# Optimization experiments

Hardware: AMD Instinct MI355X
Metric: run time of the kernel (lower is better)

Reference implementation:

```python
import jax, jax.numpy as jnp
import numpy as np

NUM_SINK = 8   # cfg.SINKHORN_ITERS
MASS = 0.9     # marginal value used for a and b


def _graph_conv(x, W_enc, b_enc, W1, b1, W2, b2, k):
    # Node encoder
    h = jax.nn.relu(x @ W_enc + b_enc)                       # [G,M,D]
    # kNN in embedding space (per graph)
    sq = jnp.sum(h * h, axis=-1)                             # [G,M]
    d2 = sq[:, :, None] + sq[:, None, :] - 2.0 * jnp.einsum('gmd,gnd->gmn', h, h)
    d2 = d2 + jnp.eye(h.shape[1], dtype=h.dtype) * 1e9       # exclude self-loop
    _, idx = jax.lax.top_k(-d2, k)                           # [G,M,k]
    neigh = jax.vmap(lambda hg, ig: hg[ig])(h, idx)          # [G,M,k,D]
    hc = jnp.broadcast_to(h[:, :, None, :], neigh.shape)
    e = jnp.concatenate([hc, neigh - hc], axis=-1)           # [G,M,k,2D]
    e = jax.nn.relu(e @ W1 + b1)                             # edge embed
    e = e @ W2 + b2                                          # back to D
    return jnp.max(e, axis=2)                                # max-aggregate over neighbors


def _sinkhorn(cost, lam):
    # log-domain unrolled Sinkhorn, batched over graphs; a=b=0.9 marginals
    log_p = -cost / lam                                      # [G,M,N]
    log_m = jnp.log(jnp.asarray(MASS, cost.dtype))
    for _ in range(NUM_SINK - 1):
        log_p = log_p - (jax.nn.logsumexp(log_p, axis=2, keepdims=True) - log_m)
        log_p = log_p - (jax.nn.logsumexp(log_p, axis=1, keepdims=True) - log_m)
    log_p = log_p - (jax.nn.logsumexp(log_p, axis=2, keepdims=True) - log_m)
    return jnp.exp(log_p)


def setup_inputs() -> dict:
    key = jax.random.key(0)
    ks = jax.random.split(key, 6)
    G, M, D = 64, 256, 256
    E = 256  # edge embed size
    inp = {
        'tra_x': jax.random.normal(ks[0], (G, M, D), jnp.float32),
        'det_x': jax.random.normal(ks[1], (G, M, D), jnp.float32),
        'W_enc': jax.random.normal(ks[2], (D, D), jnp.float32) / np.sqrt(D),
        'b_enc': jnp.zeros((D,), jnp.float32),
        'W1': jax.random.normal(ks[3], (2 * D, E), jnp.float32) / np.sqrt(2 * D),
        'b1': jnp.zeros((E,), jnp.float32),
        'W2': jax.random.normal(ks[4], (E, D), jnp.float32) / np.sqrt(E),
        'b2': jnp.zeros((D,), jnp.float32),
        'eplison': jnp.zeros((1,), jnp.float32),
        'k': 16,
    }
    return inp


def reference(tra_x, det_x, W_enc, b_enc, W1, b1, W2, b2, eplison, k):
    tra = _graph_conv(tra_x, W_enc, b_enc, W1, b1, W2, b2, k)  # [G,M,D]
    det = _graph_conv(det_x, W_enc, b_enc, W1, b1, W2, b2, k)  # [G,N,D]
    corr = jnp.einsum('gmd,gnd->gmn', tra, det)
    n1 = jnp.linalg.norm(tra, axis=-1)                         # [G,M]
    n2 = jnp.linalg.norm(det, axis=-1)                         # [G,N]
    cost = -corr / (n1[:, :, None] * n2[:, None, :])
    lam = jnp.exp(eplison[0]) + 0.03
    return _sinkhorn(cost, lam)                                # [G,M,N]
```

## Files before the change

### kernel.cpp

```cpp
#include <hip/hip_runtime.h>
#include <math.h>

#define NG 64
#define NM 256
#define ND 256
#define NK 16
#define NR (NG * NM)
#define NB 32

#define MASSF 0.9f

typedef _Float16 f16;
typedef __attribute__((ext_vector_type(8))) _Float16 f16x8;
typedef __attribute__((ext_vector_type(4))) _Float16 f16x4;
typedef __attribute__((ext_vector_type(4))) float f32x4;
typedef __attribute__((ext_vector_type(4))) unsigned u32x4;

static __device__ __forceinline__ unsigned pkrelu(unsigned a, unsigned b) {
  unsigned r;
  asm("v_pk_add_f16 %0, %1, %2" : "=v"(r) : "v"(a), "v"(b));
  asm("v_pk_max_f16 %0, %1, %2" : "=v"(r) : "v"(r), "v"(0u));
  return r;
}

__global__ __launch_bounds__(256) void prep_k(const float* __restrict__ W1,
                                              const float* __restrict__ b1,
                                              const float* __restrict__ W2,
                                              f16* __restrict__ w2t, f16* __restrict__ w1cat,
                                              float* __restrict__ biascat) {
  const int b = blockIdx.x, k = threadIdx.x;
  if (b < 256) {
    w2t[b * 256 + k] = (f16)W2[(size_t)k * 256 + b];
  } else {
    const int n = b - 256;
    float v;
    if (n < 256)
      v = W1[(size_t)k * 256 + n] - W1[(size_t)(k + 256) * 256 + n];
    else
      v = W1[(size_t)(k + 256) * 256 + (n - 256)];
    w1cat[(size_t)n * 256 + k] = (f16)v;
    if (k == 0) biascat[n] = (n < 256) ? b1[n] : 0.f;
  }
}

__global__ __launch_bounds__(256) void gemm_nn2_k(const float* __restrict__ A,
                                                  const float* __restrict__ B,
                                                  const float* __restrict__ bias,
                                                  float* __restrict__ C,
                                                  f16* __restrict__ Cf) {
  __shared__ float As[2][16][68];
  __shared__ float Bs[2][16][128];
  const int tid = threadIdx.x;
  const int tx = tid & 15, ty = tid >> 4;
  const int m0 = blockIdx.y * 64, n0 = blockIdx.x * 128;
  const int arow = tid >> 2, akc = (tid & 3) * 4;
  const int bkr = tid >> 4, bcc = (tid & 15) * 4;
  float4 av, bv0, bv1;
  float acc[4][8] = {};
  auto gload = [&](int k0) {
    av = *(const float4*)&A[(size_t)(m0 + arow) * 256 + k0 + akc];
    bv0 = *(const float4*)&B[(size_t)(k0 + bkr) * 256 + n0 + bcc];
    bv1 = *(const float4*)&B[(size_t)(k0 + bkr) * 256 + n0 + 64 + bcc];
  };
  auto swrite = [&](int buf) {
    As[buf][akc + 0][arow] = av.x;
    As[buf][akc + 1][arow] = av.y;
    As[buf][akc + 2][arow] = av.z;
    As[buf][akc + 3][arow] = av.w;
    *(float4*)&Bs[buf][bkr][bcc] = bv0;
    *(float4*)&Bs[buf][bkr][64 + bcc] = bv1;
  };
  gload(0);
  swrite(0);
  __syncthreads();
  for (int s = 0; s < 16; ++s) {
    if (s < 15) gload((s + 1) * 16);
    const int buf = s & 1;
#pragma unroll
    for (int kk = 0; kk < 16; ++kk) {
      const float4 a0 = *(const float4*)&As[buf][kk][ty * 4];
      const float4 b0 = *(const float4*)&Bs[buf][kk][tx * 4];
      const float4 b1 = *(const float4*)&Bs[buf][kk][64 + tx * 4];
      const float aa[4] = {a0.x, a0.y, a0.z, a0.w};
      const float bb[8] = {b0.x, b0.y, b0.z, b0.w, b1.x, b1.y, b1.z, b1.w};
#pragma unroll
      for (int i = 0; i < 4; ++i)
#pragma unroll
        for (int j = 0; j < 8; ++j) acc[i][j] = fmaf(aa[i], bb[j], acc[i][j]);
    }
    if (s < 15) swrite((s + 1) & 1);
    __syncthreads();
  }
  const float4 bia0 = *(const float4*)&bias[n0 + tx * 4];
  const float4 bia1 = *(const float4*)&bias[n0 + 64 + tx * 4];
#pragma unroll
  for (int i = 0; i < 4; ++i) {
    const size_t row = (size_t)(m0 + ty * 4 + i);
    float4 o0 = {fmaxf(acc[i][0] + bia0.x, 0.f), fmaxf(acc[i][1] + bia0.y, 0.f),
                 fmaxf(acc[i][2] + bia0.z, 0.f), fmaxf(acc[i][3] + bia0.w, 0.f)};
    float4 o1 = {fmaxf(acc[i][4] + bia1.x, 0.f), fmaxf(acc[i][5] + bia1.y, 0.f),
                 fmaxf(acc[i][6] + bia1.z, 0.f), fmaxf(acc[i][7] + bia1.w, 0.f)};
    *(float4*)&C[row * 256 + n0 + tx * 4] = o0;
    *(float4*)&C[row * 256 + n0 + 64 + tx * 4] = o1;
    f16x4 h0 = {(f16)o0.x, (f16)o0.y, (f16)o0.z, (f16)o0.w};
    f16x4 h1 = {(f16)o1.x, (f16)o1.y, (f16)o1.z, (f16)o1.w};
    *(f16x4*)&Cf[row * 256 + n0 + tx * 4] = h0;
    *(f16x4*)&Cf[row * 256 + n0 + 64 + tx * 4] = h1;
  }
}

__global__ __launch_bounds__(256) void gemm_nt2_k(const float* __restrict__ h,
                                                  float* __restrict__ C,
                                                  float* __restrict__ sq) {
  const int flat0 = blockIdx.x + 2 * (blockIdx.y + 4 * blockIdx.z);
  const int flat = ((flat0 & 7) << 6) | (flat0 >> 3);
  const int bx = flat & 1, by = (flat >> 1) & 3, g = flat >> 3;
  if (bx == 0 && by >= 2) return;
  __shared__ float As[2][16][68];
  __shared__ float Bs[2][16][128];
  const float* Ag = h + (size_t)g * NM * ND;
  float* Cg = C + (size_t)g * NM * NM;
  const int tid = threadIdx.x;
  const int tx = tid & 15, ty = tid >> 4;
  const int m0 = by * 64, n0 = bx * 128;
  const int arow = tid >> 2, akc = (tid & 3) * 4;
  const int brow = tid >> 1, bkc = (tid & 1) * 8;
  float4 av, bva, bvb;
  float acc[4][8] = {};
  auto gload = [&](int k0) {
    av = *(const float4*)&Ag[(size_t)(m0 + arow) * 256 + k0 + akc];
    bva = *(const float4*)&Ag[(size_t)(n0 + brow) * 256 + k0 + bkc];
    bvb = *(const float4*)&Ag[(size_t)(n0 + brow) * 256 + k0 + bkc + 4];
  };
  auto swrite = [&](int buf) {
    As[buf][akc + 0][arow] = av.x;
    As[buf][akc + 1][arow] = av.y;
    As[buf][akc + 2][arow] = av.z;
    As[buf][akc + 3][arow] = av.w;
    Bs[buf][bkc + 0][brow] = bva.x;
    Bs[buf][bkc + 1][brow] = bva.y;
    Bs[buf][bkc + 2][brow] = bva.z;
    Bs[buf][bkc + 3][brow] = bva.w;
    Bs[buf][bkc + 4][brow] = bvb.x;
    Bs[buf][bkc + 5][brow] = bvb.y;
    Bs[buf][bkc + 6][brow] = bvb.z;
    Bs[buf][bkc + 7][brow] = bvb.w;
  };
  gload(0);
  swrite(0);
  __syncthreads();
  for (int s = 0; s < 16; ++s) {
    if (s < 15) gload((s + 1) * 16);
    const int buf = s & 1;
#pragma unroll
    for (int kk = 0; kk < 16; ++kk) {
      const float4 a0 = *(const float4*)&As[buf][kk][ty * 4];
      const float4 b0 = *(const float4*)&Bs[buf][kk][tx * 4];
      const float4 b1 = *(const float4*)&Bs[buf][kk][64 + tx * 4];
      const float aa[4] = {a0.x, a0.y, a0.z, a0.w};
      const float bb[8] = {b0.x, b0.y, b0.z, b0.w, b1.x, b1.y, b1.z, b1.w};
#pragma unroll
      for (int i = 0; i < 4; ++i)
#pragma unroll
        for (int j = 0; j < 8; ++j) acc[i][j] = fmaf(aa[i], bb[j], acc[i][j]);
    }
    if (s < 15) swrite((s + 1) & 1);
    __syncthreads();
  }
  const int c0 = n0 + tx * 4, c1 = n0 + 64 + tx * 4;
#pragma unroll
  for (int i = 0; i < 4; ++i) {
    const int row = m0 + ty * 4 + i;
    float4 o0 = {acc[i][0], acc[i][1], acc[i][2], acc[i][3]};
    float4 o1 = {acc[i][4], acc[i][5], acc[i][6], acc[i][7]};
    *(float4*)&Cg[(size_t)row * 256 + c0] = o0;
    *(float4*)&Cg[(size_t)row * 256 + c1] = o1;
    if (row >= c0 && row < c0 + 4) sq[g * 256 + row] = acc[i][row - c0];
    if (row >= c1 && row < c1 + 4) sq[g * 256 + row] = acc[i][4 + row - c1];
  }
  if (bx == 1 && by < 2) {
#pragma unroll
    for (int j = 0; j < 4; ++j) {
      const size_t col0 = (size_t)(n0 + tx * 4 + j);
      const size_t col1 = (size_t)(n0 + 64 + tx * 4 + j);
      float4 t0 = {acc[0][j], acc[1][j], acc[2][j], acc[3][j]};
      float4 t1 = {acc[0][4 + j], acc[1][4 + j], acc[2][4 + j], acc[3][4 + j]};
      *(float4*)&Cg[col0 * 256 + m0 + ty * 4] = t0;
      *(float4*)&Cg[col1 * 256 + m0 + ty * 4] = t1;
    }
  }
}

__global__ __launch_bounds__(256, 2) void mlp1_mfma_k(const f16* __restrict__ A,
                                                      const f16* __restrict__ Bt,
                                                      const float* __restrict__ biascat,
                                                      f16* __restrict__ baseb,
                                                      f16* __restrict__ n1b) {
  __shared__ char As[64 * 512];
  const int tid = threadIdx.x;
  const int l = tid & 63, wv = tid >> 6;
  const int r = l & 15, gq = l >> 4;
  const int m0 = blockIdx.y * 64, n0 = blockIdx.x * 128;
  f16x8 bfr[2][8];
  float bv[2];
#pragma unroll
  for (int nt = 0; nt < 2; ++nt) {
    const int col = n0 + wv * 32 + nt * 16 + r;
    const f16* wb = Bt + (size_t)col * 256 + gq * 8;
#pragma unroll
    for (int ks = 0; ks < 8; ++ks) bfr[nt][ks] = *(const f16x8*)(wb + ks * 32);
    bv[nt] = biascat[col];
  }
  const int row = tid >> 2, ch = tid & 3;
  const char* ag = (const char*)(A + (size_t)(m0 + row) * 256) + ch * 128;
  char* lb = As + row * 512;
#pragma unroll
  for (int j = 0; j < 8; ++j)
    *(f16x8*)(lb + (((ch * 128 + j * 16)) ^ ((row & 7) << 4))) = *(const f16x8*)(ag + j * 16);
  __syncthreads();
  f32x4 acc[4][2];
#pragma unroll
  for (int mt = 0; mt < 4; ++mt)
#pragma unroll
    for (int nt = 0; nt < 2; ++nt) acc[mt][nt] = (f32x4){0.f, 0.f, 0.f, 0.f};
#pragma unroll
  for (int ks = 0; ks < 8; ++ks) {
    f16x8 a[4];
#pragma unroll
    for (int mt = 0; mt < 4; ++mt)
      a[mt] = *(const f16x8*)(As + (mt * 16 + r) * 512 + ((gq * 16 + ks * 64) ^ ((r & 7) << 4)));
#pragma unroll
    for (int mt = 0; mt < 4; ++mt)
#pragma unroll
      for (int nt = 0; nt < 2; ++nt)
        acc[mt][nt] = __builtin_amdgcn_mfma_f32_16x16x32_f16(a[mt], bfr[nt][ks], acc[mt][nt], 0, 0, 0);
  }
  f16* dst = (n0 < 256) ? baseb : n1b;
  const int cb = (n0 < 256) ? n0 : n0 - 256;
#pragma unroll
  for (int mt = 0; mt < 4; ++mt)
#pragma unroll
    for (int nt = 0; nt < 2; ++nt) {
      const int col = cb + wv * 32 + nt * 16 + r;
#pragma unroll
      for (int reg = 0; reg < 4; ++reg) {
        const int rw = m0 + mt * 16 + gq * 4 + reg;
        dst[(size_t)rw * 256 + col] = (f16)(acc[mt][nt][reg] + bv[nt]);
      }
    }
}

__global__ __launch_bounds__(256, 2) void cost_mfma_k(const f16* __restrict__ featT,
                                                      const f16* __restrict__ featD,
                                                      const float* __restrict__ nA,
                                                      const float* __restrict__ nB,
                                                      const float* __restrict__ eps,
                                                      float* __restrict__ P) {
  __shared__ char As[64 * 512];
  const int g = blockIdx.z;
  const f16* A = featT + (size_t)g * NM * ND;
  const f16* Bt = featD + (size_t)g * NM * ND;
  const int tid = threadIdx.x;
  const int l = tid & 63, wv = tid >> 6;
  const int r = l & 15, gq = l >> 4;
  const int m0 = blockIdx.y * 64, n0 = blockIdx.x * 128;
  f16x8 bfr[2][8];
  float rnb[2];
#pragma unroll
  for (int nt = 0; nt < 2; ++nt) {
    const int col = n0 + wv * 32 + nt * 16 + r;
    const f16* wb = Bt + (size_t)col * 256 + gq * 8;
#pragma unroll
    for (int ks = 0; ks < 8; ++ks) bfr[nt][ks] = *(const f16x8*)(wb + ks * 32);
    rnb[nt] = 1.0f / nB[g * NM + col];
  }
  const int row = tid >> 2, ch = tid & 3;
  const char* ag = (const char*)(A + (size_t)(m0 + row) * 256) + ch * 128;
  char* lb = As + row * 512;
#pragma unroll
  for (int j = 0; j < 8; ++j)
    *(f16x8*)(lb + (((ch * 128 + j * 16)) ^ ((row & 7) << 4))) = *(const f16x8*)(ag + j * 16);
  __syncthreads();
  f32x4 acc[4][2];
#pragma unroll
  for (int mt = 0; mt < 4; ++mt)
#pragma unroll
    for (int nt = 0; nt < 2; ++nt) acc[mt][nt] = (f32x4){0.f, 0.f, 0.f, 0.f};
#pragma unroll
  for (int ks = 0; ks < 8; ++ks) {
    f16x8 a[4];
#pragma unroll
    for (int mt = 0; mt < 4; ++mt)
      a[mt] = *(const f16x8*)(As + (mt * 16 + r) * 512 + ((gq * 16 + ks * 64) ^ ((r & 7) << 4)));
#pragma unroll
    for (int mt = 0; mt < 4; ++mt)
#pragma unroll
      for (int nt = 0; nt < 2; ++nt)
        acc[mt][nt] = __builtin_amdgcn_mfma_f32_16x16x32_f16(a[mt], bfr[nt][ks], acc[mt][nt], 0, 0, 0);
  }
  const float inv_lam = 1.0f / (expf(eps[0]) + 0.03f);
#pragma unroll
  for (int mt = 0; mt < 4; ++mt) {
    float ria[4];
#pragma unroll
    for (int reg = 0; reg < 4; ++reg)
      ria[reg] = inv_lam / nA[g * NM + m0 + mt * 16 + gq * 4 + reg];
#pragma unroll
    for (int nt = 0; nt < 2; ++nt) {
      const int col = n0 + wv * 32 + nt * 16 + r;
#pragma unroll
      for (int reg = 0; reg < 4; ++reg) {
        const int rw = m0 + mt * 16 + gq * 4 + reg;
        P[(size_t)g * NM * NM + (size_t)rw * 256 + col] =
            expf(acc[mt][nt][reg] * ria[reg] * rnb[nt]);
      }
    }
  }
}

__global__ __launch_bounds__(256) void topk_k(const float* __restrict__ S,
                                              const float* __restrict__ sq,
                                              int* __restrict__ idx) {
  const int w = threadIdx.x >> 6, lane = threadIdx.x & 63;
  const int row = blockIdx.x * 4 + w;
  const int g = row >> 8, m = row & 255;
  const float* Srow = S + (size_t)row * NM;
  const float* sqg = sq + g * NM;
  const float sm = sqg[m];
  const float4 sv = *(const float4*)&Srow[lane * 4];
  const float4 qv = *(const float4*)&sqg[lane * 4];
  float cand[4] = {sm + qv.x - 2.f * sv.x, sm + qv.y - 2.f * sv.y, sm + qv.z - 2.f * sv.z,
                   sm + qv.w - 2.f * sv.w};
#pragma unroll
  for (int t = 0; t < 4; ++t)
    if (lane * 4 + t == m) cand[t] = 1e30f;
  for (int rnd = 0; rnd < NK; ++rnd) {
    float bvv = cand[0];
    int bi = lane * 4;
#pragma unroll
    for (int t = 1; t < 4; ++t)
      if (cand[t] < bvv) {
        bvv = cand[t];
        bi = lane * 4 + t;
      }
#pragma unroll
    for (int off = 1; off < 64; off <<= 1) {
      const float ov = __shfl_xor(bvv, off);
      const int oi = __shfl_xor(bi, off);
      if (ov < bvv || (ov == bvv && oi < bi)) {
        bvv = ov;
        bi = oi;
      }
    }
    if (lane == 0) idx[(size_t)row * NK + rnd] = bi;
    if ((bi >> 2) == lane) cand[bi & 3] = 1e30f;
  }
}

__global__ __launch_bounds__(512, 4) void edgemlp_mfma8_k(
    const f16* __restrict__ baseb, const f16* __restrict__ n1b, const int* __restrict__ idx,
    const f16* __restrict__ w2t, const float* __restrict__ b2, f16* __restrict__ featf,
    float* __restrict__ nrm) {
  __shared__ unsigned E[2][2][512 * 4];
  __shared__ int sidx[NB * NK];
  __shared__ float normp[NB][8];
  const int tid = threadIdx.x;
  const int l = tid & 63, wv = tid >> 6;
  const int blk = ((blockIdx.x & 7) << 6) | (blockIdx.x >> 3);
  const int node0 = blk * NB;
  const int g = node0 >> 8;
  const int r = l & 15, gq = l >> 4;
  sidx[tid] = idx[(size_t)node0 * NK + tid];
  f16x8 bfr[2][8];
  float b2v[2];
#pragma unroll
  for (int t = 0; t < 2; ++t) {
    const int nb = wv * 2 + t;
    const f16* wb = w2t + (size_t)(nb * 16 + r) * 256 + gq * 8;
#pragma unroll
    for (int ks = 0; ks < 8; ++ks) bfr[t][ks] = *(const f16x8*)(wb + ks * 32);
    b2v[t] = b2[nb * 16 + r];
  }
  __syncthreads();
  const int r_s = tid & 15;
  const int col_s = ((tid >> 6) * 32) + (((tid >> 4) & 3) * 8);
  u32x4 bs0, ns0, bs1, ns1;
  auto sload = [&](int s) {
    const int na = s * 2;
    bs0 = *(const u32x4*)(baseb + (((size_t)(node0 + na)) << 8) + col_s);
    ns0 = *(const u32x4*)(n1b + ((((size_t)g << 8) + sidx[na * NK + r_s]) << 8) + col_s);
    bs1 = *(const u32x4*)(baseb + (((size_t)(node0 + na + 1)) << 8) + col_s);
    ns1 = *(const u32x4*)(n1b + ((((size_t)g << 8) + sidx[(na + 1) * NK + r_s]) << 8) + col_s);
  };
  auto swrite = [&](int s) {
    const int buf = s & 1;
    u32x4 w0, w1;
#pragma unroll
    for (int q = 0; q < 4; ++q) {
      w0[q] = pkrelu(bs0[q], ns0[q]);
      w1[q] = pkrelu(bs1[q], ns1[q]);
    }
    *(u32x4*)&E[buf][0][tid * 4] = w0;
    *(u32x4*)&E[buf][1][tid * 4] = w1;
  };
  sload(0);
  swrite(0);
  __syncthreads();
  for (int s = 0; s < NB / 2; ++s) {
    if (s + 1 < NB / 2) sload(s + 1);
    const int buf = s & 1;
#pragma unroll
    for (int q = 0; q < 2; ++q) {
      const char* eb = (const char*)&E[buf][q][0];
      f32x4 acc0 = (f32x4){0.f, 0.f, 0.f, 0.f};
      f32x4 acc1 = (f32x4){0.f, 0.f, 0.f, 0.f};
#pragma unroll
      for (int ks = 0; ks < 8; ++ks) {
        const f16x8 a = *(const f16x8*)(eb + ks * 1024 + l * 16);
        acc0 = __builtin_amdgcn_mfma_f32_16x16x32_f16(a, bfr[0][ks], acc0, 0, 0, 0);
        acc1 = __builtin_amdgcn_mfma_f32_16x16x32_f16(a, bfr[1][ks], acc1, 0, 0, 0);
      }
      const int nd = node0 + s * 2 + q;
      float m0v = fmaxf(fmaxf(acc0[0], acc0[1]), fmaxf(acc0[2], acc0[3]));
      m0v = fmaxf(m0v, __shfl_xor(m0v, 16));
      m0v = fmaxf(m0v, __shfl_xor(m0v, 32));
      float m1v = fmaxf(fmaxf(acc1[0], acc1[1]), fmaxf(acc1[2], acc1[3]));
      m1v = fmaxf(m1v, __shfl_xor(m1v, 16));
      m1v = fmaxf(m1v, __shfl_xor(m1v, 32));
      const f16 h0 = (f16)(m0v + b2v[0]);
      const f16 h1 = (f16)(m1v + b2v[1]);
      if (gq == 0) {
        featf[((size_t)nd << 8) + (wv * 2 + 0) * 16 + r] = h0;
        featf[((size_t)nd << 8) + (wv * 2 + 1) * 16 + r] = h1;
      }
      const float o0 = (float)h0, o1 = (float)h1;
      float ss = o0 * o0 + o1 * o1;
      ss += __shfl_xor(ss, 1);
      ss += __shfl_xor(ss, 2);
      ss += __shfl_xor(ss, 4);
      ss += __shfl_xor(ss, 8);
      if (l == 0) normp[s * 2 + q][wv] = ss;
    }
    if (s + 1 < NB / 2) swrite(s + 1);
    __syncthreads();
  }
  if (tid < NB) {
    float s = 0.f;
#pragma unroll
    for (int w = 0; w < 8; ++w) s += normp[tid][w];
    nrm[node0 + tid] = sqrtf(s);
  }
}

__global__ __launch_bounds__(1024) void sinkhorn_k(float* __restrict__ P) {
  __shared__ float red[16][256];
  __shared__ float scal[256];
  const int t = threadIdx.x;
  const int tc = t & 15;
  const int trw = t >> 4;
  const int wv = t >> 6, l = t & 63;
  float* Pg = P + (size_t)blockIdx.x * NM * NM;
  float p[4][16];
#pragma unroll
  for (int i = 0; i < 4; ++i)
#pragma unroll
    for (int q = 0; q < 4; ++q)
      *(f32x4*)&p[i][q * 4] = *(const f32x4*)&Pg[(size_t)(trw * 4 + i) * NM + tc * 16 + q * 4];

  auto rowpass = [&]() {
#pragma unroll
    for (int i = 0; i < 4; ++i) {
      float s = p[i][0];
#pragma unroll
      for (int j = 1; j < 16; ++j) s += p[i][j];
      s += __shfl_xor(s, 1);
      s += __shfl_xor(s, 2);
      s += __shfl_xor(s, 4);
      s += __shfl_xor(s, 8);
      const float sc = MASSF / s;
#pragma unroll
      for (int j = 0; j < 16; ++j) p[i][j] *= sc;
    }
  };
  auto colpass = [&]() {
    float tmp[16];
#pragma unroll
    for (int j = 0; j < 16; ++j) tmp[j] = ((p[0][j] + p[1][j]) + (p[2][j] + p[3][j]));
#pragma unroll
    for (int j = 0; j < 16; ++j) {
      tmp[j] += __shfl_xor(tmp[j], 16);
      tmp[j] += __shfl_xor(tmp[j], 32);
    }
    if (l < 16) {
#pragma unroll
      for (int q = 0; q < 4; ++q)
        *(f32x4*)&red[wv][l * 16 + q * 4] = *(const f32x4*)&tmp[q * 4];
    }
    __syncthreads();
    if (t < 256) {
      float s = red[0][t];
#pragma unroll
      for (int w = 1; w < 16; ++w) s += red[w][t];
      scal[t] = MASSF / s;
    }
    __syncthreads();
#pragma unroll
    for (int j = 0; j < 16; ++j) {
      const float sc = scal[tc * 16 + j];
#pragma unroll
      for (int i = 0; i < 4; ++i) p[i][j] *= sc;
    }
    __syncthreads();
  };
  for (int it = 0; it < 7; ++it) {
    rowpass();
    colpass();
  }
  rowpass();
#pragma unroll
  for (int i = 0; i < 4; ++i)
#pragma unroll
    for (int q = 0; q < 4; ++q)
      *(f32x4*)&Pg[(size_t)(trw * 4 + i) * NM + tc * 16 + q * 4] = *(const f32x4*)&p[i][q * 4];
}

extern "C" void kernel_launch(void* const* d_in, const int* in_sizes, int n_in, void* d_out,
                              int out_size, void* d_ws, size_t ws_size, hipStream_t stream) {
  const float* tra_x = (const float*)d_in[0];
  const float* det_x = (const float*)d_in[1];
  const float* W_enc = (const float*)d_in[2];
  const float* b_enc = (const float*)d_in[3];
  const float* W1 = (const float*)d_in[4];
  const float* b1 = (const float*)d_in[5];
  const float* W2 = (const float*)d_in[6];
  const float* b2 = (const float*)d_in[7];
  const float* eps = (const float*)d_in[8];
  float* out = (float*)d_out;

  const size_t SZ = (size_t)NR * ND;
  float* h = (float*)d_ws;
  f16* hf = (f16*)(h + SZ);
  f16* baseb = hf + SZ;
  f16* n1b = baseb + SZ;
  f16* featT = n1b + SZ;
  f16* featD = featT + SZ;
  float* sq = (float*)(featD + SZ);
  float* nT = sq + NR;
  float* nD = nT + NR;
  int* idx = (int*)(nD + NR);
  f16* w2t = (f16*)(idx + (size_t)NR * NK);
  f16* w1cat = w2t + 256 * 256;
  float* biascat = (float*)(w1cat + 512 * 256);
  float* S = out;

  const float* xs[2] = {tra_x, det_x};
  f16* feats[2] = {featT, featD};
  float* nrms[2] = {nT, nD};

  prep_k<<<768, 256, 0, stream>>>(W1, b1, W2, w2t, w1cat, biascat);
  for (int s2 = 0; s2 < 2; ++s2) {
    gemm_nn2_k<<<dim3(2, 256), 256, 0, stream>>>(xs[s2], W_enc, b_enc, h, hf);
    mlp1_mfma_k<<<dim3(4, 256), 256, 0, stream>>>(hf, w1cat, biascat, baseb, n1b);
    gemm_nt2_k<<<dim3(2, 4, NG), 256, 0, stream>>>(h, S, sq);
    topk_k<<<4096, 256, 0, stream>>>(S, sq, idx);
    edgemlp_mfma8_k<<<NR / NB, 512, 0, stream>>>(baseb, n1b, idx, w2t, b2, feats[s2], nrms[s2]);
  }
  cost_mfma_k<<<dim3(2, 4, NG), 256, 0, stream>>>(featT, featD, nT, nD, eps, out);
  sinkhorn_k<<<NG, 1024, 0, stream>>>(out);
}
```

Before: 377.7 us.

## Halve edge-MLP block to 4 waves with 4 column tiles each; swizzle cost grid

The edge-MLP kernel now runs 256 threads instead of 512. Each wave holds four W2 column tiles in registers instead of two, so every LDS A-fragment load feeds four MFMAs rather than two. Each thread also loads twice as many gathered edge elements per stage. The cost kernel switches to a flat 1D grid with an XCD-style swizzle so that blocks of the same graph land together. The edge-MLP change raises register pressure (64 VGPRs of B fragments) and lowers the thread count per block, which could hurt latency hiding.

```diff
diff --git a/kernel.cpp b/kernel.cpp
--- a/kernel.cpp
+++ b/kernel.cpp
@@ -257,13 +257,14 @@
                                                       const float* __restrict__ eps,
                                                       float* __restrict__ P) {
   __shared__ char As[64 * 512];
-  const int g = blockIdx.z;
+  const int flat = ((blockIdx.x & 7) << 6) | (blockIdx.x >> 3);
+  const int bx = flat & 1, by = (flat >> 1) & 3, g = flat >> 3;
   const f16* A = featT + (size_t)g * NM * ND;
   const f16* Bt = featD + (size_t)g * NM * ND;
   const int tid = threadIdx.x;
   const int l = tid & 63, wv = tid >> 6;
   const int r = l & 15, gq = l >> 4;
-  const int m0 = blockIdx.y * 64, n0 = blockIdx.x * 128;
+  const int m0 = by * 64, n0 = bx * 128;
   f16x8 bfr[2][8];
   float rnb[2];
 #pragma unroll
@@ -357,13 +358,13 @@
   }
 }
 
-__global__ __launch_bounds__(512, 4) void edgemlp_mfma8_k(
+__global__ __launch_bounds__(256, 2) void edgemlp_mfma9_k(
     const f16* __restrict__ baseb, const f16* __restrict__ n1b, const int* __restrict__ idx,
     const f16* __restrict__ w2t, const float* __restrict__ b2, f16* __restrict__ featf,
     float* __restrict__ nrm) {
   __shared__ unsigned E[2][2][512 * 4];
   __shared__ int sidx[NB * NK];
-  __shared__ float normp[NB][8];
+  __shared__ float normp[NB][4];
   const int tid = threadIdx.x;
   const int l = tid & 63, wv = tid >> 6;
   const int blk = ((blockIdx.x & 7) << 6) | (blockIdx.x >> 3);
@@ -371,11 +372,12 @@
   const int g = node0 >> 8;
   const int r = l & 15, gq = l >> 4;
   sidx[tid] = idx[(size_t)node0 * NK + tid];
-  f16x8 bfr[2][8];
-  float b2v[2];
-#pragma unroll
-  for (int t = 0; t < 2; ++t) {
-    const int nb = wv * 2 + t;
+  sidx[tid + 256] = idx[(size_t)node0 * NK + tid + 256];
+  f16x8 bfr[4][8];
+  float b2v[4];
+#pragma unroll
+  for (int t = 0; t < 4; ++t) {
+    const int nb = wv * 4 + t;
     const f16* wb = w2t + (size_t)(nb * 16 + r) * 256 + gq * 8;
 #pragma unroll
     for (int ks = 0; ks < 8; ++ks) bfr[t][ks] = *(const f16x8*)(wb + ks * 32);
@@ -384,24 +386,36 @@
   __syncthreads();
   const int r_s = tid & 15;
   const int col_s = ((tid >> 6) * 32) + (((tid >> 4) & 3) * 8);
-  u32x4 bs0, ns0, bs1, ns1;
+  u32x4 ba0, ba1, na0, na1, bb0, bb1, nb0v, nb1v;
   auto sload = [&](int s) {
     const int na = s * 2;
-    bs0 = *(const u32x4*)(baseb + (((size_t)(node0 + na)) << 8) + col_s);
-    ns0 = *(const u32x4*)(n1b + ((((size_t)g << 8) + sidx[na * NK + r_s]) << 8) + col_s);
-    bs1 = *(const u32x4*)(baseb + (((size_t)(node0 + na + 1)) << 8) + col_s);
-    ns1 = *(const u32x4*)(n1b + ((((size_t)g << 8) + sidx[(na + 1) * NK + r_s]) << 8) + col_s);
+    const f16* pa = baseb + (((size_t)(node0 + na)) << 8);
+    const f16* qa = n1b + ((((size_t)g << 8) + sidx[na * NK + r_s]) << 8);
+    ba0 = *(const u32x4*)(pa + col_s);
+    ba1 = *(const u32x4*)(pa + col_s + 128);
+    na0 = *(const u32x4*)(qa + col_s);
+    na1 = *(const u32x4*)(qa + col_s + 128);
+    const f16* pb = baseb + (((size_t)(node0 + na + 1)) << 8);
+    const f16* qb = n1b + ((((size_t)g << 8) + sidx[(na + 1) * NK + r_s]) << 8);
+    bb0 = *(const u32x4*)(pb + col_s);
+    bb1 = *(const u32x4*)(pb + col_s + 128);
+    nb0v = *(const u32x4*)(qb + col_s);
+    nb1v = *(const u32x4*)(qb + col_s + 128);
   };
   auto swrite = [&](int s) {
     const int buf = s & 1;
-    u32x4 w0, w1;
+    u32x4 w0, w1, w2, w3;
 #pragma unroll
     for (int q = 0; q < 4; ++q) {
-      w0[q] = pkrelu(bs0[q], ns0[q]);
-      w1[q] = pkrelu(bs1[q], ns1[q]);
+      w0[q] = pkrelu(ba0[q], na0[q]);
+      w1[q] = pkrelu(ba1[q], na1[q]);
+      w2[q] = pkrelu(bb0[q], nb0v[q]);
+      w3[q] = pkrelu(bb1[q], nb1v[q]);
     }
     *(u32x4*)&E[buf][0][tid * 4] = w0;
-    *(u32x4*)&E[buf][1][tid * 4] = w1;
+    *(u32x4*)&E[buf][0][(tid + 256) * 4] = w1;
+    *(u32x4*)&E[buf][1][tid * 4] = w2;
+    *(u32x4*)&E[buf][1][(tid + 256) * 4] = w3;
   };
   sload(0);
   swrite(0);
@@ -412,29 +426,32 @@
 #pragma unroll
     for (int q = 0; q < 2; ++q) {
       const char* eb = (const char*)&E[buf][q][0];
-      f32x4 acc0 = (f32x4){0.f, 0.f, 0.f, 0.f};
-      f32x4 acc1 = (f32x4){0.f, 0.f, 0.f, 0.f};
+      f32x4 acc[4];
+#pragma unroll
+      for (int t = 0; t < 4; ++t) acc[t] = (f32x4){0.f, 0.f, 0.f, 0.f};
 #pragma unroll
       for (int ks = 0; ks < 8; ++ks) {
         const f16x8 a = *(const f16x8*)(eb + ks * 1024 + l * 16);
-        acc0 = __builtin_amdgcn_mfma_f32_16x16x32_f16(a, bfr[0][ks], acc0, 0, 0, 0);
-        acc1 = __builtin_amdgcn_mfma_f32_16x16x32_f16(a, bfr[1][ks], acc1, 0, 0, 0);
+#pragma unroll
+        for (int t = 0; t < 4; ++t)
+          acc[t] = __builtin_amdgcn_mfma_f32_16x16x32_f16(a, bfr[t][ks], acc[t], 0, 0, 0);
       }
       const int nd = node0 + s * 2 + q;
-      float m0v = fmaxf(fmaxf(acc0[0], acc0[1]), fmaxf(acc0[2], acc0[3]));
-      m0v = fmaxf(m0v, __shfl_xor(m0v, 16));
-      m0v = fmaxf(m0v, __shfl_xor(m0v, 32));
-      float m1v = fmaxf(fmaxf(acc1[0], acc1[1]), fmaxf(acc1[2], acc1[3]));
-      m1v = fmaxf(m1v, __shfl_xor(m1v, 16));
-      m1v = fmaxf(m1v, __shfl_xor(m1v, 32));
-      const f16 h0 = (f16)(m0v + b2v[0]);
-      const f16 h1 = (f16)(m1v + b2v[1]);
+      float ss = 0.f;
+      f16 hv[4];
+#pragma unroll
+      for (int t = 0; t < 4; ++t) {
+        float m1 = fmaxf(fmaxf(acc[t][0], acc[t][1]), fmaxf(acc[t][2], acc[t][3]));
+        m1 = fmaxf(m1, __shfl_xor(m1, 16));
+        m1 = fmaxf(m1, __shfl_xor(m1, 32));
+        hv[t] = (f16)(m1 + b2v[t]);
+        const float o = (float)hv[t];
+        ss += o * o;
+      }
       if (gq == 0) {
-        featf[((size_t)nd << 8) + (wv * 2 + 0) * 16 + r] = h0;
-        featf[((size_t)nd << 8) + (wv * 2 + 1) * 16 + r] = h1;
-      }
-      const float o0 = (float)h0, o1 = (float)h1;
-      float ss = o0 * o0 + o1 * o1;
+#pragma unroll
+        for (int t = 0; t < 4; ++t) featf[((size_t)nd << 8) + (wv * 4 + t) * 16 + r] = hv[t];
+      }
       ss += __shfl_xor(ss, 1);
       ss += __shfl_xor(ss, 2);
       ss += __shfl_xor(ss, 4);
@@ -445,9 +462,7 @@
     __syncthreads();
   }
   if (tid < NB) {
-    float s = 0.f;
-#pragma unroll
-    for (int w = 0; w < 8; ++w) s += normp[tid][w];
+    float s = normp[tid][0] + normp[tid][1] + normp[tid][2] + normp[tid][3];
     nrm[node0 + tid] = sqrtf(s);
   }
 }
@@ -563,8 +578,8 @@
     mlp1_mfma_k<<<dim3(4, 256), 256, 0, stream>>>(hf, w1cat, biascat, baseb, n1b);
     gemm_nt2_k<<<dim3(2, 4, NG), 256, 0, stream>>>(h, S, sq);
     topk_k<<<4096, 256, 0, stream>>>(S, sq, idx);
-    edgemlp_mfma8_k<<<NR / NB, 512, 0, stream>>>(baseb, n1b, idx, w2t, b2, feats[s2], nrms[s2]);
-  }
-  cost_mfma_k<<<dim3(2, 4, NG), 256, 0, stream>>>(featT, featD, nT, nD, eps, out);
+    edgemlp_mfma9_k<<<NR / NB, 256, 0, stream>>>(baseb, n1b, idx, w2t, b2, feats[s2], nrms[s2]);
+  }
+  cost_mfma_k<<<512, 256, 0, stream>>>(featT, featD, nT, nD, eps, out);
   sinkhorn_k<<<NG, 1024, 0, stream>>>(out);
 }
```

After: 385.0 us. About the same (+1.9%).

## Batch both graph-conv edge MLPs into one launch and swizzle cost grid

Applied to the files above, without the earlier changes.

Workspace buffers for baseb, n1b and idx are doubled so both the tra and det branches keep their intermediates. The edge-MLP kernel then runs once over a 1024-block grid covering both halves instead of twice with 512 blocks each. The cost kernel switches from a 3D grid to a flat grid with an XCD-style block index swizzle, so blocks of the same graph group together. This removes one launch and gives a larger grid for occupancy, at the cost of more workspace memory.

```diff
diff --git a/kernel.cpp b/kernel.cpp
--- a/kernel.cpp
+++ b/kernel.cpp
@@ -257,13 +257,14 @@
                                                       const float* __restrict__ eps,
                                                       float* __restrict__ P) {
   __shared__ char As[64 * 512];
-  const int g = blockIdx.z;
+  const int flat = ((blockIdx.x & 7) << 6) | (blockIdx.x >> 3);
+  const int bx = flat & 1, by = (flat >> 1) & 3, g = flat >> 3;
   const f16* A = featT + (size_t)g * NM * ND;
   const f16* Bt = featD + (size_t)g * NM * ND;
   const int tid = threadIdx.x;
   const int l = tid & 63, wv = tid >> 6;
   const int r = l & 15, gq = l >> 4;
-  const int m0 = blockIdx.y * 64, n0 = blockIdx.x * 128;
+  const int m0 = by * 64, n0 = bx * 128;
   f16x8 bfr[2][8];
   float rnb[2];
 #pragma unroll
@@ -357,18 +358,27 @@
   }
 }
 
-__global__ __launch_bounds__(512, 4) void edgemlp_mfma8_k(
-    const f16* __restrict__ baseb, const f16* __restrict__ n1b, const int* __restrict__ idx,
-    const f16* __restrict__ w2t, const float* __restrict__ b2, f16* __restrict__ featf,
-    float* __restrict__ nrm) {
+__global__ __launch_bounds__(512, 4) void edgemlp_mfma10_k(
+    const f16* __restrict__ baseb2, const f16* __restrict__ n1b2, const int* __restrict__ idx2,
+    const f16* __restrict__ w2t, const float* __restrict__ b2, f16* __restrict__ featf2,
+    float* __restrict__ nrm2) {
   __shared__ unsigned E[2][2][512 * 4];
   __shared__ int sidx[NB * NK];
   __shared__ float normp[NB][8];
   const int tid = threadIdx.x;
   const int l = tid & 63, wv = tid >> 6;
-  const int blk = ((blockIdx.x & 7) << 6) | (blockIdx.x >> 3);
+  const size_t SZH = (size_t)NR * ND;
+  const int bid = blockIdx.x;
+  const int half = bid >> 9;
+  const int b9 = bid & 511;
+  const int blk = ((b9 & 7) << 6) | (b9 >> 3);
   const int node0 = blk * NB;
   const int g = node0 >> 8;
+  const f16* baseb = baseb2 + (size_t)half * SZH;
+  const f16* n1b = n1b2 + (size_t)half * SZH;
+  const int* idx = idx2 + (size_t)half * NR * NK;
+  f16* featf = featf2 + (size_t)half * SZH;
+  float* nrm = nrm2 + (size_t)half * NR;
   const int r = l & 15, gq = l >> 4;
   sidx[tid] = idx[(size_t)node0 * NK + tid];
   f16x8 bfr[2][8];
@@ -541,30 +551,29 @@
   float* h = (float*)d_ws;
   f16* hf = (f16*)(h + SZ);
   f16* baseb = hf + SZ;
-  f16* n1b = baseb + SZ;
-  f16* featT = n1b + SZ;
+  f16* n1b = baseb + 2 * SZ;
+  f16* featT = n1b + 2 * SZ;
   f16* featD = featT + SZ;
   float* sq = (float*)(featD + SZ);
   float* nT = sq + NR;
   float* nD = nT + NR;
   int* idx = (int*)(nD + NR);
-  f16* w2t = (f16*)(idx + (size_t)NR * NK);
+  f16* w2t = (f16*)(idx + 2 * (size_t)NR * NK);
   f16* w1cat = w2t + 256 * 256;
   float* biascat = (float*)(w1cat + 512 * 256);
   float* S = out;
 
   const float* xs[2] = {tra_x, det_x};
-  f16* feats[2] = {featT, featD};
-  float* nrms[2] = {nT, nD};
 
   prep_k<<<768, 256, 0, stream>>>(W1, b1, W2, w2t, w1cat, biascat);
   for (int s2 = 0; s2 < 2; ++s2) {
     gemm_nn2_k<<<dim3(2, 256), 256, 0, stream>>>(xs[s2], W_enc, b_enc, h, hf);
-    mlp1_mfma_k<<<dim3(4, 256), 256, 0, stream>>>(hf, w1cat, biascat, baseb, n1b);
+    mlp1_mfma_k<<<dim3(4, 256), 256, 0, stream>>>(hf, w1cat, biascat, baseb + s2 * SZ,
+                                                  n1b + s2 * SZ);
     gemm_nt2_k<<<dim3(2, 4, NG), 256, 0, stream>>>(h, S, sq);
-    topk_k<<<4096, 256, 0, stream>>>(S, sq, idx);
-    edgemlp_mfma8_k<<<NR / NB, 512, 0, stream>>>(baseb, n1b, idx, w2t, b2, feats[s2], nrms[s2]);
-  }
-  cost_mfma_k<<<dim3(2, 4, NG), 256, 0, stream>>>(featT, featD, nT, nD, eps, out);
+    topk_k<<<4096, 256, 0, stream>>>(S, sq, idx + (size_t)s2 * NR * NK);
+  }
+  edgemlp_mfma10_k<<<1024, 512, 0, stream>>>(baseb, n1b, idx, w2t, b2, featT, nT);
+  cost_mfma_k<<<512, 256, 0, stream>>>(featT, featD, nT, nD, eps, out);
   sinkhorn_k<<<NG, 1024, 0, stream>>>(out);
 }
```

New measurement: 371.7 us. No clear change (-1.6%).
